# Kernel tuning notes

Hardware: AMD Instinct MI355X
Metric: run time of the kernel (lower is better)

## Reference

```python
import jax, jax.numpy as jnp
import numpy as np

H = 128        # hidden_dim
R = 50         # num_rbf
L = 4          # num_layers
CUTOFF = 5.0
N = 10000      # atoms
M = 64         # molecules
BOX = 54.7     # box side -> ~32 neighbors within cutoff
EPS = 1e-5     # LayerNorm eps (torch default)


def setup_inputs() -> dict:
    rng = np.random.default_rng(0)
    positions = rng.uniform(0.0, BOX, size=(N, 3)).astype(np.float32)
    # static radius graph (the torch module filters a dense NxN pair list by cutoff;
    # we do that once here so runtime shapes are fixed / jit-friendly)
    sq = (positions ** 2).sum(-1)
    d2 = sq[:, None] + sq[None, :] - 2.0 * positions @ positions.T
    mask = (d2 < CUTOFF * CUTOFF) & ~np.eye(N, dtype=bool)
    row, col = np.nonzero(mask)
    edge_index = jnp.asarray(np.stack([row, col]).astype(np.int32))  # [2, E]

    key = jax.random.key(0)
    ks = jax.random.split(key, 6)
    s = 0.05
    return dict(
        atomic_numbers=jax.random.randint(ks[0], (N,), 0, 100),
        positions=jnp.asarray(positions),
        batch=jnp.asarray((np.arange(N) * M // N).astype(np.int32)),  # sorted, all M present
        edge_index=edge_index,
        embedding=jax.random.normal(ks[1], (100, H), jnp.float32) * s,
        W1=jax.random.normal(ks[2], (L, H + R, H), jnp.float32) * s,
        b1=jnp.zeros((L, H), jnp.float32),
        W2=jax.random.normal(ks[3], (L, H, H), jnp.float32) * s,
        b2=jnp.zeros((L, H), jnp.float32),
        W_ih=jax.random.normal(ks[4], (L, H, 3 * H), jnp.float32) * s,
        b_ih=jax.random.normal(ks[5], (L, 3 * H), jnp.float32) * s,
        b_hh=jnp.zeros((L, 3 * H), jnp.float32),
        ln_g=jnp.ones((H,), jnp.float32),
        ln_b=jnp.zeros((H,), jnp.float32),
    )


def reference(atomic_numbers, positions, batch, edge_index, embedding,
              W1, b1, W2, b2, W_ih, b_ih, b_hh, ln_g, ln_b):
    x = embedding[jnp.clip(atomic_numbers, 0, 99)]                  # [N, H]
    row, col = edge_index[0], edge_index[1]
    d = jnp.linalg.norm(positions[row] - positions[col], axis=-1)   # [E]
    centers = jnp.linspace(0.0, CUTOFF, R)
    width = CUTOFF / R
    rbf = jnp.exp(-((d[:, None] - centers) ** 2) / (2.0 * width * width))  # [E, R]
    n_atoms = x.shape[0]
    for l in range(L):
        x_j = x[row]                                                # gather [E, H]
        inp = jnp.concatenate([x_j, rbf], axis=-1)                  # [E, H+R]
        msg = jax.nn.silu(inp @ W1[l] + b1[l]) @ W2[l] + b2[l]      # [E, H]
        aggr = jax.ops.segment_sum(msg, col, num_segments=n_atoms)  # [N, H]
        # GRU step with h0 = 0: W_hh @ h vanishes, only b_hh survives
        gi = aggr @ W_ih[l] + b_ih[l]                               # [N, 3H]
        gi_r, gi_z, gi_n = jnp.split(gi, 3, axis=-1)
        bh_r, bh_z, bh_n = jnp.split(b_hh[l], 3)
        r = jax.nn.sigmoid(gi_r + bh_r)
        z = jax.nn.sigmoid(gi_z + bh_z)
        n = jnp.tanh(gi_n + r * bh_n)
        x = x + (1.0 - z) * n                                       # h' = (1-z)*n + z*0
    mu = x.mean(-1, keepdims=True)
    var = ((x - mu) ** 2).mean(-1, keepdims=True)
    x = (x - mu) / jnp.sqrt(var + EPS) * ln_g + ln_b
    sums = jax.ops.segment_sum(x, batch, num_segments=M)            # [M, H]
    counts = jax.ops.segment_sum(jnp.ones((x.shape[0],), jnp.float32), batch, num_segments=M)
    graph_rep = sums / jnp.clip(counts, 1.0)[:, None]
    return x, graph_rep
```

## Files before the change

kernel.cpp:

```cpp
#include <hip/hip_runtime.h>
#include <hip/hip_bf16.h>
#include <math.h>


#define HH 128
#define RR 50
#define LL 4
#define L2E 1.4426950408889634f

typedef __attribute__((ext_vector_type(8))) short short8;
typedef __attribute__((ext_vector_type(4))) float floatx4;

__device__ __forceinline__ unsigned short f2bf(float f) {
    unsigned u = __float_as_uint(f);
    unsigned r = (u + 0x7fffu + ((u >> 16) & 1u)) >> 16;
    return (unsigned short)r;
}
__device__ __forceinline__ unsigned pack_bf2(float lo, float hi) {
    unsigned u0 = __float_as_uint(lo) + 0x8000u;
    unsigned u1 = __float_as_uint(hi) + 0x8000u;
    return __builtin_amdgcn_perm(u1, u0, 0x07060302);
}
__device__ __forceinline__ float fast_sigmoid(float x) {
    return __builtin_amdgcn_rcpf(1.f + __builtin_amdgcn_exp2f(x * (-L2E)));
}
__device__ __forceinline__ float fast_tanh(float x) {
    x = fminf(fmaxf(x, -15.f), 15.f);
    float t = __builtin_amdgcn_exp2f(x * (2.f * L2E));
    return (t - 1.f) * __builtin_amdgcn_rcpf(t + 1.f);
}
__device__ __forceinline__ int imin(int a, int b) { return a < b ? a : b; }

__global__ __launch_bounds__(256) void prep_kernel(
    const int* __restrict__ an, const float* __restrict__ emb,
    float* __restrict__ X,
    const float* __restrict__ pos, const int* __restrict__ erow,
    const int* __restrict__ ecol, float* __restrict__ dist,
    int* __restrict__ rowptr, int* __restrict__ bptr,
    const int* __restrict__ batch,
    const float* __restrict__ W1, unsigned short* __restrict__ W1rT,
    unsigned short* __restrict__ W1xT,
    const float* __restrict__ W2, const float* __restrict__ Wih,
    unsigned short* __restrict__ WcT,
    const float* __restrict__ b2, float* __restrict__ P,
    int N, int E, int M)
{
    int gidx = blockIdx.x * 256 + threadIdx.x;
    int c0 = N * HH;
    if (gidx < c0) {
        int i = gidx >> 7, n = gidx & 127;
        int z = an[i];
        z = z < 0 ? 0 : (z > 99 ? 99 : z);
        X[gidx] = emb[z * HH + n];
        return;
    }
    gidx -= c0;
    int PT = E > N ? E : N;
    if (gidx < PT) {
        int i = gidx;
        if (i < E) {
            int rc = erow[i];
            int rp = (i > 0) ? erow[i - 1] : -1;
            for (int r = rp + 1; r <= rc; ++r) rowptr[r] = i;
            if (i == E - 1)
                for (int r = rc + 1; r <= N; ++r) rowptr[r] = E;
        }
        if (i < N) {
            int bc = batch[i];
            int bp = (i > 0) ? batch[i - 1] : -1;
            for (int m = bp + 1; m <= bc; ++m) bptr[m] = i;
            if (i == N - 1)
                for (int m = bc + 1; m <= M; ++m) bptr[m] = N;
        }
        return;
    }
    gidx -= PT;
    if (gidx < E) {
        int e = gidx;
        int r = erow[e], c = ecol[e];
        float dx = pos[r * 3 + 0] - pos[c * 3 + 0];
        float dy = pos[r * 3 + 1] - pos[c * 3 + 1];
        float dz = pos[r * 3 + 2] - pos[c * 3 + 2];
        dist[e] = sqrtf(dx * dx + dy * dy + dz * dz);
        return;
    }
    gidx -= E;
    if (gidx < LL * HH * 64) {
        int l = gidx >> 13, rem = gidx & 8191;
        int f = rem >> 9, lane2 = (rem >> 3) & 63, j = rem & 7;
        int nt = f >> 1, h = f & 1;
        int n = nt * 16 + (lane2 & 15);
        int k = h * 32 + (lane2 >> 4) * 8 + j;
        float v = (k < RR) ? W1[((size_t)l * 178 + 128 + k) * HH + n] : 0.f;
        W1rT[gidx] = f2bf(v);
        return;
    }
    gidx -= LL * HH * 64;
    if (gidx < LL * HH * HH) {
        int l = gidx >> 14, rem = gidx & 16383, n = rem >> 7, k = rem & 127;
        W1xT[gidx] = f2bf(W1[((size_t)l * 178 + k) * HH + n]);
        return;
    }
    gidx -= LL * HH * HH;
    if (gidx < LL * HH * 384) {
        int l = gidx / (HH * 384), rem = gidx % (HH * 384);
        int i = rem / 384, j = rem % 384;
        const float* w2row = W2 + ((size_t)l * HH + i) * HH;
        const float* wih = Wih + (size_t)l * HH * 384;
        float acc = 0.f;
#pragma unroll 4
        for (int k = 0; k < HH; ++k)
            acc = fmaf(w2row[k], wih[(size_t)k * 384 + j], acc);
        WcT[((size_t)l * 384 + j) * HH + i] = f2bf(acc);
        return;
    }
    gidx -= LL * HH * 384;
    if (gidx < LL * 384) {
        int l = gidx / 384, j = gidx % 384;
        const float* b2l = b2 + (size_t)l * HH;
        const float* wih = Wih + (size_t)l * HH * 384;
        float acc = 0.f;
#pragma unroll 4
        for (int k = 0; k < HH; ++k)
            acc = fmaf(b2l[k], wih[(size_t)k * 384 + j], acc);
        P[gidx] = acc;
    }
}

#define XAB 32
__global__ __launch_bounds__(256) void xw_kernel(
    const float* __restrict__ X, const float* __restrict__ W,
    const float* __restrict__ bias, unsigned short* __restrict__ XWb, int N)
{
    __shared__ __align__(16) float A[XAB][HH];
    int tid = threadIdx.x;
    int abase = blockIdx.x * XAB;
    for (int idx = tid; idx < XAB * HH; idx += 256) {
        int a = idx >> 7, k = idx & 127;
        A[a][k] = (abase + a < N) ? X[(size_t)(abase + a) * HH + k] : 0.f;
    }
    __syncthreads();
    int n = tid & 127, s = tid >> 7;
    float acc[16];
#pragma unroll
    for (int i = 0; i < 16; ++i) acc[i] = 0.f;
    for (int kc = 0; kc < 32; ++kc) {
        float w0 = W[(4 * kc + 0) * HH + n];
        float w1 = W[(4 * kc + 1) * HH + n];
        float w2 = W[(4 * kc + 2) * HH + n];
        float w3 = W[(4 * kc + 3) * HH + n];
#pragma unroll
        for (int i = 0; i < 16; ++i) {
            float4 av = *(const float4*)&A[s * 16 + i][4 * kc];
            acc[i] = fmaf(av.x, w0, acc[i]);
            acc[i] = fmaf(av.y, w1, acc[i]);
            acc[i] = fmaf(av.z, w2, acc[i]);
            acc[i] = fmaf(av.w, w3, acc[i]);
        }
    }
    float b = bias[n];
#pragma unroll
    for (int i = 0; i < 16; ++i) {
        int a = abase + s * 16 + i;
        if (a < N) XWb[(size_t)a * HH + n] = f2bf(acc[i] + b);
    }
}

__global__ __launch_bounds__(256) void edge_mfma_kernel(
    const unsigned short* __restrict__ XWb, const unsigned short* __restrict__ W1rTf,
    const float* __restrict__ dist, const int* __restrict__ rowptr,
    const int* __restrict__ ecol, unsigned short* __restrict__ Sbf,
    int N, int nwaves)
{
    __shared__ __align__(16) unsigned short W1s[8192];
    int tid = threadIdx.x;
    {
        const uint4* src = (const uint4*)W1rTf;
        uint4* dst = (uint4*)W1s;
#pragma unroll
        for (int i = 0; i < 4; ++i) dst[tid + i * 256] = src[tid + i * 256];
    }
    __syncthreads();

    int wid = (blockIdx.x << 2) + (tid >> 6);
    int lane = tid & 63;
    int c = lane & 15, q = lane >> 4;

    const float stepc = 5.0f / 49.0f;
    const float negc = -50.f * L2E;
    float kqs = (float)(q << 3) * stepc;

    for (int a = wid; a < N; a += nwaves) {
        int es = rowptr[a], ee = rowptr[a + 1];
        float acc[8][4];
#pragma unroll
        for (int nt = 0; nt < 8; ++nt)
#pragma unroll
            for (int r = 0; r < 4; ++r) acc[nt][r] = 0.f;

        if (es < ee) {
            int last = ee - 1;
            int ce0 = imin(es + c, last);
            float dcur = dist[ce0];
            int colcur = ecol[ce0];
            int ce1 = imin(es + 16 + c, last);
            float dnxt = dist[ce1];
            int colnxt = ecol[ce1];

            for (int eb = es; eb < ee; eb += 16) {
                const unsigned short* xwrow = XWb + (size_t)colcur * HH;
                uint2 gx[8];
#pragma unroll
                for (int nt = 0; nt < 8; ++nt)
                    gx[nt] = *(const uint2*)&xwrow[nt * 16 + (q << 2)];

                float d_t = dcur;
                dcur = dnxt; colcur = colnxt;
                int ce2 = imin(eb + 32 + c, last);
                dnxt = dist[ce2];
                colnxt = ecol[ce2];

                float dq0 = d_t - kqs;
                float dq1 = dq0 - 32.f * stepc;
                union { unsigned u[4]; short8 s; } ub0, ub1;
#pragma unroll
                for (int p = 0; p < 4; ++p) {
                    float t0 = dq0 - (float)(2 * p) * stepc;
                    float t1 = dq0 - (float)(2 * p + 1) * stepc;
                    float e0 = __builtin_amdgcn_exp2f(negc * t0 * t0);
                    float e1 = __builtin_amdgcn_exp2f(negc * t1 * t1);
                    ub0.u[p] = pack_bf2(e0, e1);
                    float t2 = dq1 - (float)(2 * p) * stepc;
                    float t3 = dq1 - (float)(2 * p + 1) * stepc;
                    float e2 = __builtin_amdgcn_exp2f(negc * t2 * t2);
                    float e3 = __builtin_amdgcn_exp2f(negc * t3 * t3);
                    ub1.u[p] = pack_bf2(e2, e3);
                }
                short8 B0 = ub0.s, B1 = ub1.s;
                float msk = ((eb + c) < ee) ? 1.f : 0.f;

                unsigned wbyte = (unsigned)(lane * 16);
                asm volatile("" : "+v"(wbyte));
                const char* Wlp = (const char*)W1s + wbyte;

#pragma unroll
                for (int nt = 0; nt < 8; ++nt) {
                    short8 A0 = *(const short8*)(Wlp + (nt * 2 + 0) * 1024);
                    short8 A1 = *(const short8*)(Wlp + (nt * 2 + 1) * 1024);
                    floatx4 C;
                    C[0] = __uint_as_float(gx[nt].x << 16);
                    C[1] = __uint_as_float(gx[nt].x & 0xffff0000u);
                    C[2] = __uint_as_float(gx[nt].y << 16);
                    C[3] = __uint_as_float(gx[nt].y & 0xffff0000u);
                    C = __builtin_amdgcn_mfma_f32_16x16x32_bf16(A0, B0, C, 0, 0, 0);
                    C = __builtin_amdgcn_mfma_f32_16x16x32_bf16(A1, B1, C, 0, 0, 0);
#pragma unroll
                    for (int r = 0; r < 4; ++r) {
                        float h = C[r];
                        float v = h * fast_sigmoid(h);
                        acc[nt][r] = fmaf(v, msk, acc[nt][r]);
                    }
                }
            }
        }

        int b3 = (c >> 3) & 1, b0 = c & 1, b1 = (c >> 1) & 1, b2 = (c >> 2) & 1;
        float s16[8][2];
#pragma unroll
        for (int t = 0; t < 8; ++t)
#pragma unroll
            for (int p = 0; p < 2; ++p) {
                float keep = b3 ? acc[t][2 + p] : acc[t][p];
                float send = b3 ? acc[t][p] : acc[t][2 + p];
                s16[t][p] = keep + __shfl_xor(send, 8, 64);
            }
        float s8[4][2];
#pragma unroll
        for (int t = 0; t < 4; ++t)
#pragma unroll
            for (int p = 0; p < 2; ++p) {
                float keep = b0 ? s16[2 * t + 1][p] : s16[2 * t][p];
                float send = b0 ? s16[2 * t][p] : s16[2 * t + 1][p];
                s8[t][p] = keep + __shfl_xor(send, 1, 64);
            }
        float s4[2][2];
#pragma unroll
        for (int u = 0; u < 2; ++u)
#pragma unroll
            for (int p = 0; p < 2; ++p) {
                float keep = b1 ? s8[2 * u + 1][p] : s8[2 * u][p];
                float send = b1 ? s8[2 * u][p] : s8[2 * u + 1][p];
                s4[u][p] = keep + __shfl_xor(send, 2, 64);
            }
        float s2[2];
#pragma unroll
        for (int p = 0; p < 2; ++p) {
            float keep = b2 ? s4[1][p] : s4[0][p];
            float send = b2 ? s4[0][p] : s4[1][p];
            s2[p] = keep + __shfl_xor(send, 4, 64);
        }
        unsigned pk = pack_bf2(s2[0], s2[1]);
        *(unsigned*)&Sbf[(size_t)a * HH + (c & 7) * 16 + (q << 2) + (b3 << 1)] = pk;
    }
}

#define GA 32
__global__ __launch_bounds__(256) void grux_mfma_kernel(
    const unsigned short* __restrict__ Sbf, const unsigned short* __restrict__ WcT,
    const float* __restrict__ P, const float* __restrict__ bih,
    const float* __restrict__ bhh, const int* __restrict__ rowptr,
    float* __restrict__ X, int N,
    const unsigned short* __restrict__ W1xT, const float* __restrict__ b1next,
    unsigned short* __restrict__ XWb, int do_xw)
{
    __shared__ __align__(16) unsigned short Sb[GA][136];
    __shared__ __align__(16) unsigned short Xb[GA][136];
    int tid = threadIdx.x;
    int abase = blockIdx.x * GA;
    int w = tid >> 6, lane = tid & 63, c = lane & 15, q = lane >> 4;

    float pn[2][3], bi[2][3], bh[2][3], deg[2][4];
#pragma unroll
    for (int t = 0; t < 2; ++t) {
        int n = w * 32 + t * 16 + c;
#pragma unroll
        for (int g = 0; g < 3; ++g) {
            pn[t][g] = P[g * 128 + n];
            bi[t][g] = bih[g * 128 + n];
            bh[t][g] = bhh[g * 128 + n];
        }
    }
#pragma unroll
    for (int sub = 0; sub < 2; ++sub)
#pragma unroll
        for (int r = 0; r < 4; ++r) {
            int a = abase + sub * 16 + q * 4 + r;
            deg[sub][r] = (a < N) ? (float)(rowptr[a + 1] - rowptr[a]) : 0.f;
        }

    {
        int a = tid >> 3, ch = tid & 7;
        int aa = abase + a; if (aa >= N) aa = N - 1;
        const uint4* src = (const uint4*)(Sbf + (size_t)aa * HH + ch * 16);
        uint4 v0 = src[0];
        uint4 v1 = src[1];
        uint4* dst = (uint4*)&Sb[a][ch * 16];
        dst[0] = v0;
        dst[1] = v1;
    }
    __syncthreads();

    floatx4 Cg[3][2][2];
#pragma unroll
    for (int g = 0; g < 3; ++g)
#pragma unroll
        for (int t = 0; t < 2; ++t)
#pragma unroll
            for (int sub = 0; sub < 2; ++sub)
                Cg[g][t][sub] = floatx4{0.f, 0.f, 0.f, 0.f};

#pragma unroll
    for (int kt = 0; kt < 4; ++kt) {
        short8 A0 = *(const short8*)&Sb[c][kt * 32 + q * 8];
        short8 A1 = *(const short8*)&Sb[16 + c][kt * 32 + q * 8];
#pragma unroll
        for (int g = 0; g < 3; ++g)
#pragma unroll
            for (int t = 0; t < 2; ++t) {
                int nrow = g * 128 + w * 32 + t * 16 + c;
                short8 B = *(const short8*)&WcT[(size_t)nrow * HH + kt * 32 + q * 8];
                Cg[g][t][0] = __builtin_amdgcn_mfma_f32_16x16x32_bf16(A0, B, Cg[g][t][0], 0, 0, 0);
                Cg[g][t][1] = __builtin_amdgcn_mfma_f32_16x16x32_bf16(A1, B, Cg[g][t][1], 0, 0, 0);
            }
    }

#pragma unroll
    for (int sub = 0; sub < 2; ++sub)
#pragma unroll
        for (int r = 0; r < 4; ++r) {
            int am = sub * 16 + q * 4 + r;
            int a = abase + am;
            bool ok = a < N;
#pragma unroll
            for (int t = 0; t < 2; ++t) {
                int n = w * 32 + t * 16 + c;
                float g0 = Cg[0][t][sub][r] + deg[sub][r] * pn[t][0] + bi[t][0];
                float g1 = Cg[1][t][sub][r] + deg[sub][r] * pn[t][1] + bi[t][1];
                float g2 = Cg[2][t][sub][r] + deg[sub][r] * pn[t][2] + bi[t][2];
                float rr = fast_sigmoid(g0 + bh[t][0]);
                float zz = fast_sigmoid(g1 + bh[t][1]);
                float nn = fast_tanh(g2 + rr * bh[t][2]);
                float xv = 0.f;
                if (ok) {
                    xv = X[(size_t)a * HH + n] + (1.f - zz) * nn;
                    X[(size_t)a * HH + n] = xv;
                }
                Xb[am][n] = f2bf(xv);
            }
        }

    if (!do_xw) return;
    __syncthreads();

    floatx4 Cx[2][2];
#pragma unroll
    for (int t = 0; t < 2; ++t)
#pragma unroll
        for (int sub = 0; sub < 2; ++sub)
            Cx[t][sub] = floatx4{0.f, 0.f, 0.f, 0.f};
#pragma unroll
    for (int kt = 0; kt < 4; ++kt) {
        short8 A0 = *(const short8*)&Xb[c][kt * 32 + q * 8];
        short8 A1 = *(const short8*)&Xb[16 + c][kt * 32 + q * 8];
#pragma unroll
        for (int t = 0; t < 2; ++t) {
            int nrow = w * 32 + t * 16 + c;
            short8 B = *(const short8*)&W1xT[(size_t)nrow * HH + kt * 32 + q * 8];
            Cx[t][0] = __builtin_amdgcn_mfma_f32_16x16x32_bf16(A0, B, Cx[t][0], 0, 0, 0);
            Cx[t][1] = __builtin_amdgcn_mfma_f32_16x16x32_bf16(A1, B, Cx[t][1], 0, 0, 0);
        }
    }
#pragma unroll
    for (int sub = 0; sub < 2; ++sub)
#pragma unroll
        for (int r = 0; r < 4; ++r) {
            int a = abase + sub * 16 + q * 4 + r;
            if (a >= N) continue;
#pragma unroll
            for (int t = 0; t < 2; ++t) {
                int n = w * 32 + t * 16 + c;
                XWb[(size_t)a * HH + n] = f2bf(Cx[t][sub][r] + b1next[n]);
            }
        }
}

__global__ __launch_bounds__(256) void ln_kernel(
    const float* __restrict__ X, const float* __restrict__ g,
    const float* __restrict__ b, float* __restrict__ out, int N)
{
    int a = blockIdx.x * 4 + (threadIdx.x >> 6);
    int lane = threadIdx.x & 63;
    if (a >= N) return;
    float v0 = X[(size_t)a * HH + lane];
    float v1 = X[(size_t)a * HH + 64 + lane];
    float sm = v0 + v1;
    for (int off = 32; off > 0; off >>= 1) sm += __shfl_xor(sm, off, 64);
    float mu = sm * (1.f / 128.f);
    float d0 = v0 - mu, d1 = v1 - mu;
    float vq = d0 * d0 + d1 * d1;
    for (int off = 32; off > 0; off >>= 1) vq += __shfl_xor(vq, off, 64);
    float inv = rsqrtf(vq * (1.f / 128.f) + 1e-5f);
    out[(size_t)a * HH + lane] = d0 * inv * g[lane] + b[lane];
    out[(size_t)a * HH + 64 + lane] = d1 * inv * g[64 + lane] + b[64 + lane];
}

__global__ __launch_bounds__(256) void pool_kernel(
    const float* __restrict__ outx, const int* __restrict__ bptr,
    float* __restrict__ outg)
{
    __shared__ float sm[256];
    int m = blockIdx.x, t = threadIdx.x;
    int n = t & 127, s = t >> 7;
    int a0 = bptr[m], a1 = bptr[m + 1];
    float acc = 0.f;
    for (int a = a0 + s; a < a1; a += 2)
        acc += outx[(size_t)a * HH + n];
    sm[t] = acc;
    __syncthreads();
    if (t < 128) {
        float cnt = (float)(a1 - a0);
        outg[(size_t)m * HH + t] = (sm[t] + sm[t + 128]) / fmaxf(cnt, 1.f);
    }
}

extern "C" void kernel_launch(void* const* d_in, const int* in_sizes, int n_in,
                              void* d_out, int out_size, void* d_ws, size_t ws_size,
                              hipStream_t stream)
{
    const int*   an   = (const int*)d_in[0];
    const float* pos  = (const float*)d_in[1];
    const int*   bat  = (const int*)d_in[2];
    const int*   eidx = (const int*)d_in[3];
    const float* emb  = (const float*)d_in[4];
    const float* W1   = (const float*)d_in[5];
    const float* b1   = (const float*)d_in[6];
    const float* W2   = (const float*)d_in[7];
    const float* b2   = (const float*)d_in[8];
    const float* Wih  = (const float*)d_in[9];
    const float* bih  = (const float*)d_in[10];
    const float* bhh  = (const float*)d_in[11];
    const float* lng  = (const float*)d_in[12];
    const float* lnb  = (const float*)d_in[13];

    int N = in_sizes[0];
    int E = in_sizes[3] / 2;
    int M = out_size / HH - N;
    const int* erow = eidx;
    const int* ecol = eidx + E;

    float* ws   = (float*)d_ws;
    size_t off = 0;
    float* X    = ws + off; off += (size_t)N * HH;
    unsigned short* Sbf = (unsigned short*)(ws + off); off += (size_t)N * HH / 2;
    unsigned short* XWb = (unsigned short*)(ws + off); off += (size_t)N * HH / 2;
    float* P    = ws + off; off += LL * 384;
    float* dist = ws + off; off += E;
    int* rowptr = (int*)(ws + off); off += N + 1;
    int* bptr   = (int*)(ws + off); off += M + 1;
    off = (off + 3) & ~(size_t)3;
    unsigned short* W1rT = (unsigned short*)(ws + off); off += (size_t)LL * HH * 32;
    unsigned short* W1xT = (unsigned short*)(ws + off); off += (size_t)LL * HH * 64;
    unsigned short* WcT  = (unsigned short*)(ws + off); off += (size_t)LL * 384 * 64;

    float* outx = (float*)d_out;
    float* outg = outx + (size_t)N * HH;

    int PT = (E > N ? E : N);
    long total = (long)N * HH + PT + E + LL * HH * 64 + LL * HH * HH
               + LL * HH * 384 + LL * 384;
    int prep_blocks = (int)((total + 255) / 256);

    prep_kernel<<<prep_blocks, 256, 0, stream>>>(
        an, emb, X, pos, erow, ecol, dist, rowptr, bptr, bat,
        W1, W1rT, W1xT, W2, Wih, WcT, b2, P, N, E, M);

    xw_kernel<<<(N + XAB - 1) / XAB, 256, 0, stream>>>(X, W1, b1, XWb, N);

    int eblocks = (N + 3) / 4;
    int nwaves = eblocks * 4;
    int grux_blocks = (N + GA - 1) / GA;
    for (int l = 0; l < LL; ++l) {
        edge_mfma_kernel<<<eblocks, 256, 0, stream>>>(
            XWb, W1rT + (size_t)l * HH * 64, dist, rowptr, ecol, Sbf, N, nwaves);
        int do_xw = (l < LL - 1) ? 1 : 0;
        int ln = (l + 1 < LL) ? l + 1 : l;
        grux_mfma_kernel<<<grux_blocks, 256, 0, stream>>>(
            Sbf, WcT + (size_t)l * 384 * HH, P + l * 384,
            bih + l * 384, bhh + l * 384, rowptr, X, N,
            W1xT + (size_t)ln * HH * HH, b1 + (size_t)ln * HH, XWb, do_xw);
    }

    ln_kernel<<<(N + 3) / 4, 256, 0, stream>>>(X, lng, lnb, outx, N);
    pool_kernel<<<M, 256, 0, stream>>>(outx, bptr, outg);
}
```

Measured before the change: 326.6 us.

## Split edge kernel hidden dim across two waves per atom; fuse LayerNorm with pooling

Result: faster. 315.3 us (median of 2 runs) (-3.5%).

```diff
diff --git a/kernel.cpp b/kernel.cpp
--- a/kernel.cpp
+++ b/kernel.cpp
@@ -190,13 +190,15 @@
     const float negc = -50.f * L2E;
     float kqs = (float)(q << 3) * stepc;
 
-    for (int a = wid; a < N; a += nwaves) {
+    int NW = 2 * N;
+    for (int w = wid; w < NW; w += nwaves) {
+        int a = w >> 1, h = w & 1;
         int es = rowptr[a], ee = rowptr[a + 1];
-        float acc[8][4];
-#pragma unroll
-        for (int nt = 0; nt < 8; ++nt)
-#pragma unroll
-            for (int r = 0; r < 4; ++r) acc[nt][r] = 0.f;
+        float acc[4][4];
+#pragma unroll
+        for (int t = 0; t < 4; ++t)
+#pragma unroll
+            for (int r = 0; r < 4; ++r) acc[t][r] = 0.f;
 
         if (es < ee) {
             int last = ee - 1;
@@ -208,11 +210,11 @@
             int colnxt = ecol[ce1];
 
             for (int eb = es; eb < ee; eb += 16) {
-                const unsigned short* xwrow = XWb + (size_t)colcur * HH;
-                uint2 gx[8];
-#pragma unroll
-                for (int nt = 0; nt < 8; ++nt)
-                    gx[nt] = *(const uint2*)&xwrow[nt * 16 + (q << 2)];
+                const unsigned short* xwrow = XWb + (size_t)colcur * HH + h * 64;
+                uint2 gx[4];
+#pragma unroll
+                for (int t = 0; t < 4; ++t)
+                    gx[t] = *(const uint2*)&xwrow[t * 16 + (q << 2)];
 
                 float d_t = dcur;
                 dcur = dnxt; colcur = colnxt;
@@ -227,14 +229,14 @@
                 for (int p = 0; p < 4; ++p) {
                     float t0 = dq0 - (float)(2 * p) * stepc;
                     float t1 = dq0 - (float)(2 * p + 1) * stepc;
-                    float e0 = __builtin_amdgcn_exp2f(negc * t0 * t0);
-                    float e1 = __builtin_amdgcn_exp2f(negc * t1 * t1);
-                    ub0.u[p] = pack_bf2(e0, e1);
+                    float e0f = __builtin_amdgcn_exp2f(negc * t0 * t0);
+                    float e1f = __builtin_amdgcn_exp2f(negc * t1 * t1);
+                    ub0.u[p] = pack_bf2(e0f, e1f);
                     float t2 = dq1 - (float)(2 * p) * stepc;
                     float t3 = dq1 - (float)(2 * p + 1) * stepc;
-                    float e2 = __builtin_amdgcn_exp2f(negc * t2 * t2);
-                    float e3 = __builtin_amdgcn_exp2f(negc * t3 * t3);
-                    ub1.u[p] = pack_bf2(e2, e3);
+                    float e2f = __builtin_amdgcn_exp2f(negc * t2 * t2);
+                    float e3f = __builtin_amdgcn_exp2f(negc * t3 * t3);
+                    ub1.u[p] = pack_bf2(e2f, e3f);
                 }
                 short8 B0 = ub0.s, B1 = ub1.s;
                 float msk = ((eb + c) < ee) ? 1.f : 0.f;
@@ -244,63 +246,59 @@
                 const char* Wlp = (const char*)W1s + wbyte;
 
 #pragma unroll
-                for (int nt = 0; nt < 8; ++nt) {
-                    short8 A0 = *(const short8*)(Wlp + (nt * 2 + 0) * 1024);
-                    short8 A1 = *(const short8*)(Wlp + (nt * 2 + 1) * 1024);
+                for (int t = 0; t < 4; ++t) {
+                    int f0 = (h * 4 + t) * 2;
+                    short8 A0 = *(const short8*)(Wlp + f0 * 1024);
+                    short8 A1 = *(const short8*)(Wlp + (f0 + 1) * 1024);
                     floatx4 C;
-                    C[0] = __uint_as_float(gx[nt].x << 16);
-                    C[1] = __uint_as_float(gx[nt].x & 0xffff0000u);
-                    C[2] = __uint_as_float(gx[nt].y << 16);
-                    C[3] = __uint_as_float(gx[nt].y & 0xffff0000u);
+                    C[0] = __uint_as_float(gx[t].x << 16);
+                    C[1] = __uint_as_float(gx[t].x & 0xffff0000u);
+                    C[2] = __uint_as_float(gx[t].y << 16);
+                    C[3] = __uint_as_float(gx[t].y & 0xffff0000u);
                     C = __builtin_amdgcn_mfma_f32_16x16x32_bf16(A0, B0, C, 0, 0, 0);
                     C = __builtin_amdgcn_mfma_f32_16x16x32_bf16(A1, B1, C, 0, 0, 0);
 #pragma unroll
                     for (int r = 0; r < 4; ++r) {
-                        float h = C[r];
-                        float v = h * fast_sigmoid(h);
-                        acc[nt][r] = fmaf(v, msk, acc[nt][r]);
+                        float hh = C[r];
+                        float v = hh * fast_sigmoid(hh);
+                        acc[t][r] = fmaf(v, msk, acc[t][r]);
                     }
                 }
             }
         }
 
-        int b3 = (c >> 3) & 1, b0 = c & 1, b1 = (c >> 1) & 1, b2 = (c >> 2) & 1;
-        float s16[8][2];
-#pragma unroll
-        for (int t = 0; t < 8; ++t)
+        int b0 = c & 1, b1 = (c >> 1) & 1, b2 = (c >> 2) & 1, b3 = (c >> 3) & 1;
+        float s1[4][2];
+#pragma unroll
+        for (int t = 0; t < 4; ++t)
 #pragma unroll
             for (int p = 0; p < 2; ++p) {
-                float keep = b3 ? acc[t][2 + p] : acc[t][p];
-                float send = b3 ? acc[t][p] : acc[t][2 + p];
-                s16[t][p] = keep + __shfl_xor(send, 8, 64);
+                float keep = b0 ? acc[t][2 * p + 1] : acc[t][2 * p];
+                float send = b0 ? acc[t][2 * p] : acc[t][2 * p + 1];
+                s1[t][p] = keep + __shfl_xor(send, 1, 64);
             }
-        float s8[4][2];
-#pragma unroll
-        for (int t = 0; t < 4; ++t)
-#pragma unroll
-            for (int p = 0; p < 2; ++p) {
-                float keep = b0 ? s16[2 * t + 1][p] : s16[2 * t][p];
-                float send = b0 ? s16[2 * t][p] : s16[2 * t + 1][p];
-                s8[t][p] = keep + __shfl_xor(send, 1, 64);
-            }
-        float s4[2][2];
-#pragma unroll
-        for (int u = 0; u < 2; ++u)
-#pragma unroll
-            for (int p = 0; p < 2; ++p) {
-                float keep = b1 ? s8[2 * u + 1][p] : s8[2 * u][p];
-                float send = b1 ? s8[2 * u][p] : s8[2 * u + 1][p];
-                s4[u][p] = keep + __shfl_xor(send, 2, 64);
-            }
-        float s2[2];
-#pragma unroll
-        for (int p = 0; p < 2; ++p) {
-            float keep = b2 ? s4[1][p] : s4[0][p];
-            float send = b2 ? s4[0][p] : s4[1][p];
-            s2[p] = keep + __shfl_xor(send, 4, 64);
-        }
-        unsigned pk = pack_bf2(s2[0], s2[1]);
-        *(unsigned*)&Sbf[(size_t)a * HH + (c & 7) * 16 + (q << 2) + (b3 << 1)] = pk;
+        float s2[4];
+#pragma unroll
+        for (int t = 0; t < 4; ++t) {
+            float keep = b1 ? s1[t][1] : s1[t][0];
+            float send = b1 ? s1[t][0] : s1[t][1];
+            s2[t] = keep + __shfl_xor(send, 2, 64);
+        }
+        float s3[2];
+#pragma unroll
+        for (int u = 0; u < 2; ++u) {
+            float keep = b2 ? s2[2 * u + 1] : s2[2 * u];
+            float send = b2 ? s2[2 * u] : s2[2 * u + 1];
+            s3[u] = keep + __shfl_xor(send, 4, 64);
+        }
+        float keep = b3 ? s3[1] : s3[0];
+        float send = b3 ? s3[0] : s3[1];
+        float fin = keep + __shfl_xor(send, 8, 64);
+
+        int t_fin = 2 * b3 + b2;
+        int r_fin = 2 * b1 + b0;
+        int n = t_fin * 16 + (q << 2) + r_fin;
+        Sbf[(size_t)a * HH + h * 64 + n] = f2bf(fin);
     }
 }
 
@@ -434,42 +432,44 @@
         }
 }
 
-__global__ __launch_bounds__(256) void ln_kernel(
+__global__ __launch_bounds__(1024) void lnpool_kernel(
     const float* __restrict__ X, const float* __restrict__ g,
-    const float* __restrict__ b, float* __restrict__ out, int N)
+    const float* __restrict__ b, const int* __restrict__ bptr,
+    float* __restrict__ outx, float* __restrict__ outg, int N)
 {
-    int a = blockIdx.x * 4 + (threadIdx.x >> 6);
-    int lane = threadIdx.x & 63;
-    if (a >= N) return;
-    float v0 = X[(size_t)a * HH + lane];
-    float v1 = X[(size_t)a * HH + 64 + lane];
-    float sm = v0 + v1;
-    for (int off = 32; off > 0; off >>= 1) sm += __shfl_xor(sm, off, 64);
-    float mu = sm * (1.f / 128.f);
-    float d0 = v0 - mu, d1 = v1 - mu;
-    float vq = d0 * d0 + d1 * d1;
-    for (int off = 32; off > 0; off >>= 1) vq += __shfl_xor(vq, off, 64);
-    float inv = rsqrtf(vq * (1.f / 128.f) + 1e-5f);
-    out[(size_t)a * HH + lane] = d0 * inv * g[lane] + b[lane];
-    out[(size_t)a * HH + 64 + lane] = d1 * inv * g[64 + lane] + b[64 + lane];
-}
-
-__global__ __launch_bounds__(256) void pool_kernel(
-    const float* __restrict__ outx, const int* __restrict__ bptr,
-    float* __restrict__ outg)
-{
-    __shared__ float sm[256];
-    int m = blockIdx.x, t = threadIdx.x;
-    int n = t & 127, s = t >> 7;
+    __shared__ float sm[16][128];
+    int m = blockIdx.x, tid = threadIdx.x;
+    int wv = tid >> 6, lane = tid & 63;
     int a0 = bptr[m], a1 = bptr[m + 1];
-    float acc = 0.f;
-    for (int a = a0 + s; a < a1; a += 2)
-        acc += outx[(size_t)a * HH + n];
-    sm[t] = acc;
+    float g0 = g[lane], g1 = g[64 + lane];
+    float bb0 = b[lane], bb1 = b[64 + lane];
+    float acc0 = 0.f, acc1 = 0.f;
+    for (int a = a0 + wv; a < a1; a += 16) {
+        float v0 = X[(size_t)a * HH + lane];
+        float v1 = X[(size_t)a * HH + 64 + lane];
+        float smv = v0 + v1;
+        for (int off = 32; off > 0; off >>= 1) smv += __shfl_xor(smv, off, 64);
+        float mu = smv * (1.f / 128.f);
+        float d0 = v0 - mu, d1 = v1 - mu;
+        float vq = d0 * d0 + d1 * d1;
+        for (int off = 32; off > 0; off >>= 1) vq += __shfl_xor(vq, off, 64);
+        float inv = rsqrtf(vq * (1.f / 128.f) + 1e-5f);
+        float y0 = d0 * inv * g0 + bb0;
+        float y1 = d1 * inv * g1 + bb1;
+        outx[(size_t)a * HH + lane] = y0;
+        outx[(size_t)a * HH + 64 + lane] = y1;
+        acc0 += y0;
+        acc1 += y1;
+    }
+    sm[wv][lane] = acc0;
+    sm[wv][64 + lane] = acc1;
     __syncthreads();
-    if (t < 128) {
+    if (tid < 128) {
+        float s = 0.f;
+#pragma unroll
+        for (int i = 0; i < 16; ++i) s += sm[i][tid];
         float cnt = (float)(a1 - a0);
-        outg[(size_t)m * HH + t] = (sm[t] + sm[t + 128]) / fmaxf(cnt, 1.f);
+        outg[(size_t)m * HH + tid] = s / fmaxf(cnt, 1.f);
     }
 }
 
@@ -526,7 +526,7 @@
 
     xw_kernel<<<(N + XAB - 1) / XAB, 256, 0, stream>>>(X, W1, b1, XWb, N);
 
-    int eblocks = (N + 3) / 4;
+    int eblocks = (2 * N + 3) / 4;
     int nwaves = eblocks * 4;
     int grux_blocks = (N + GA - 1) / GA;
     for (int l = 0; l < LL; ++l) {
@@ -540,6 +540,5 @@
             W1xT + (size_t)ln * HH * HH, b1 + (size_t)ln * HH, XWb, do_xw);
     }
 
-    ln_kernel<<<(N + 3) / 4, 256, 0, stream>>>(X, lng, lnb, outx, N);
-    pool_kernel<<<M, 256, 0, stream>>>(outx, bptr, outg);
-}
+    lnpool_kernel<<<M, 1024, 0, stream>>>(X, lng, lnb, bptr, outx, outg, N);
+}
```
